# Kernel tuning notes

Measured on AMD Instinct MI355X. Metric: run time of the kernel, lower is better.

The kernel has to match this reference:

```python
import jax, jax.numpy as jnp
import numpy as np


def setup_inputs() -> dict:
    key = jax.random.key(0)
    ks = jax.random.split(key, 7)
    B, T, D, H, DK, S = 16, 1, 4096, 32, 128, 2048
    return {
        "x": jax.random.normal(ks[0], (B, T, D), dtype=jnp.float32),
        "k_cache": jax.random.normal(ks[1], (B, H, S, DK), dtype=jnp.float32),
        "v_cache": jax.random.normal(ks[2], (B, H, S, DK), dtype=jnp.float32),
        "Wq": jax.random.normal(ks[3], (D, D), dtype=jnp.float32) * (D ** -0.5),
        "Wk": jax.random.normal(ks[4], (D, D), dtype=jnp.float32) * (D ** -0.5),
        "Wv": jax.random.normal(ks[5], (D, D), dtype=jnp.float32) * (D ** -0.5),
        "Wo": jax.random.normal(ks[6], (D, D), dtype=jnp.float32) * (D ** -0.5),
        "start_pos": 2047,
    }


def reference(x, k_cache, v_cache, Wq, Wk, Wv, Wo, start_pos):
    B, T, D = x.shape
    H, DK = k_cache.shape[1], k_cache.shape[3]
    end_pos = start_pos + T

    # QKV projections (nn.Linear with bias=False: y = x @ W.T), split heads -> (B, H, T, DK)
    def proj(W):
        return (x @ W.T).reshape(B, T, H, DK).transpose(0, 2, 1, 3)

    q = proj(Wq)
    k_new = proj(Wk)
    v_new = proj(Wv)

    # Scatter new K/V into the pre-allocated cache at start_pos (static slice)
    k_cache = jax.lax.dynamic_update_slice(k_cache, k_new, (0, 0, start_pos, 0))
    v_cache = jax.lax.dynamic_update_slice(v_cache, v_new, (0, 0, start_pos, 0))

    # Gather cached K/V up to end_pos
    k_all = k_cache[:, :, :end_pos]  # (B, H, end_pos, DK)
    v_all = v_cache[:, :, :end_pos]

    # Scaled dot-product attention with causal mask over cache positions
    scores = jnp.einsum("bhtd,bhsd->bhts", q, k_all) / jnp.sqrt(jnp.float32(DK))
    pos_q = start_pos + jnp.arange(T)          # query absolute positions
    pos_k = jnp.arange(end_pos)                # key absolute positions
    mask = pos_k[None, :] <= pos_q[:, None]    # (T, end_pos)
    scores = jnp.where(mask[None, None], scores, jnp.float32(-1e30))
    attn = jax.nn.softmax(scores, axis=-1)
    out = jnp.einsum("bhts,bhsd->bhtd", attn, v_all)

    # Merge heads and output projection
    out = out.transpose(0, 2, 1, 3).reshape(B, T, D)
    return out @ Wo.T
```

## Files before the change

### kernel.cpp

```cpp
#include <hip/hip_runtime.h>
#include <math.h>

constexpr int B  = 16;
constexpr int H  = 32;
constexpr int S  = 2048;
constexpr int DK = 128;
constexpr int D  = 4096;
constexpr int BH = B * H;

constexpr int NSPLIT = 4;
constexpr int CHUNK  = S / NSPLIT;
constexpr int NREC   = NSPLIT * 4;
constexpr int REC    = 132;

__device__ __forceinline__ float reduce64(float v[64], int lane) {
    #pragma unroll
    for (int s = 0; s < 6; ++s) {
        const int off = 1 << s;
        #pragma unroll
        for (int j = 0; j < (64 >> (s + 1)); ++j) {
            const float lo = v[2 * j], hi = v[2 * j + 1];
            const bool  up = (lane & off) != 0;
            const float mine = up ? hi : lo;
            const float oth  = up ? lo : hi;
            v[j] = mine + __shfl_xor(oth, off, 64);
        }
    }
    return v[0];
}

__global__ __launch_bounds__(256, 3) void proj_qkv_kernel(
    const float* __restrict__ X,
    const float* __restrict__ W0,
    const float* __restrict__ W1,
    const float* __restrict__ W2,
    float* __restrict__ Y0,
    float* __restrict__ Y1,
    float* __restrict__ Y2)
{
    __shared__ float4 xs[2][16][64];

    const int t    = threadIdx.x;
    const int lane = t & 63;
    const int wid  = t >> 6;
    const int tb   = t >> 4;
    const int tf   = t & 15;

    const int c0   = blockIdx.x * 16 + wid * 4;
    const int wsel = c0 >> 12;
    const int n0   = c0 & (D - 1);

    const float* Wp = (wsel == 0) ? W0 : (wsel == 1) ? W1 : W2;
    float*       Yp = (wsel == 0) ? Y0 : (wsel == 1) ? Y1 : Y2;
    const float4* w4 = (const float4*)Wp;
    const float4* x4 = (const float4*)X;

    float acc[64];
    #pragma unroll
    for (int i = 0; i < 64; ++i) acc[i] = 0.f;

    float4 xr[4];
    #pragma unroll
    for (int i = 0; i < 4; ++i) xr[i] = x4[tb * 1024 + tf + 16 * i];
    float4 wv[4];
    #pragma unroll
    for (int c = 0; c < 4; ++c) wv[c] = w4[(size_t)(n0 + c) * 1024 + lane];
    #pragma unroll
    for (int i = 0; i < 4; ++i) xs[0][tb][tf + 16 * i] = xr[i];
    __syncthreads();

    for (int ch = 0; ch < 16; ++ch) {
        float4 xn[4], wn[4];
        const bool more = (ch < 15);
        if (more) {
            #pragma unroll
            for (int i = 0; i < 4; ++i)
                xn[i] = x4[tb * 1024 + (ch + 1) * 64 + tf + 16 * i];
            #pragma unroll
            for (int c = 0; c < 4; ++c)
                wn[c] = w4[(size_t)(n0 + c) * 1024 + (ch + 1) * 64 + lane];
        }
        const int buf = ch & 1;
        #pragma unroll
        for (int b = 0; b < 16; ++b) {
            const float4 xv = xs[buf][b][lane];
            #pragma unroll
            for (int c = 0; c < 4; ++c)
                acc[b * 4 + c] += xv.x * wv[c].x + xv.y * wv[c].y +
                                  xv.z * wv[c].z + xv.w * wv[c].w;
        }
        if (more) {
            #pragma unroll
            for (int i = 0; i < 4; ++i) xs[buf ^ 1][tb][tf + 16 * i] = xn[i];
            __syncthreads();
            #pragma unroll
            for (int c = 0; c < 4; ++c) wv[c] = wn[c];
        }
    }

    const float outv = reduce64(acc, lane);
    Yp[(size_t)(lane >> 2) * D + n0 + (lane & 3)] = outv;
}

__global__ __launch_bounds__(256) void proj_wo_kernel(
    const float* __restrict__ X,
    const float* __restrict__ Wo,
    float* __restrict__ out)
{
    __shared__ float red[4][64];
    const int lane = threadIdx.x & 63;
    const int wid  = threadIdx.x >> 6;
    const int n0   = blockIdx.x * 4;
    const float4* w4 = (const float4*)Wo;
    const float4* x4 = (const float4*)X;

    float acc[64];
    #pragma unroll
    for (int i = 0; i < 64; ++i) acc[i] = 0.f;

    #pragma unroll
    for (int it = 0; it < 4; ++it) {
        const int d4 = wid * 256 + it * 64 + lane;
        float4 wv[4];
        #pragma unroll
        for (int c = 0; c < 4; ++c) wv[c] = w4[(size_t)(n0 + c) * 1024 + d4];
        #pragma unroll
        for (int b = 0; b < 16; ++b) {
            const float4 xv = x4[b * 1024 + d4];
            #pragma unroll
            for (int c = 0; c < 4; ++c)
                acc[b * 4 + c] += xv.x * wv[c].x + xv.y * wv[c].y +
                                  xv.z * wv[c].z + xv.w * wv[c].w;
        }
    }

    const float pv = reduce64(acc, lane);
    red[wid][lane] = pv;
    __syncthreads();
    if (wid == 0) {
        const float tot = red[0][lane] + red[1][lane] + red[2][lane] + red[3][lane];
        out[(size_t)(lane >> 2) * D + n0 + (lane & 3)] = tot;
    }
}

__global__ __launch_bounds__(256) void attn_kernel(
    const float* __restrict__ q,
    const float* __restrict__ k_cache,
    const float* __restrict__ v_cache,
    const float* __restrict__ k_new,
    const float* __restrict__ v_new,
    const int*   __restrict__ start_pos_p,
    float* __restrict__ part)
{
    const int lane  = threadIdx.x & 63;
    const int wid   = threadIdx.x >> 6;
    const int half  = lane >> 5;
    const int hl    = lane & 31;
    const int bh    = blockIdx.x & (BH - 1);
    const int split = blockIdx.x >> 9;

    const int sp    = start_pos_p[0];
    const int s0    = split * CHUNK;
    const int lim   = sp + 1;
    const int s_end = (s0 + CHUNK < lim) ? (s0 + CHUNK) : lim;

    const float qscale = 0.08838834764831845f * 1.4426950408889634f;
    const float shift  = 8.0f * 1.4426950408889634f;
    float4 qv = *(const float4*)(q + (size_t)bh * DK + 4 * hl);
    qv.x *= qscale; qv.y *= qscale; qv.z *= qscale; qv.w *= qscale;

    const float* kbase = k_cache + (size_t)bh * S * DK;
    const float* vbase = v_cache + (size_t)bh * S * DK;
    const float* knew  = k_new + (size_t)bh * DK;
    const float* vnew  = v_new + (size_t)bh * DK;

    float  l = 0.f;
    float4 acc = make_float4(0.f, 0.f, 0.f, 0.f);

    #pragma unroll 2
    for (int s2 = s0 + 2 * wid; s2 < s_end; s2 += 8) {
        const int  pos   = s2 + half;
        const bool valid = pos < s_end;
        const int  cpos  = valid ? pos : (s_end - 1);
        const float* kp = (cpos == sp) ? knew : (kbase + (size_t)cpos * DK);
        const float* vp = (cpos == sp) ? vnew : (vbase + (size_t)cpos * DK);
        const float4 kv = *(const float4*)(kp + 4 * hl);
        const float4 vv = *(const float4*)(vp + 4 * hl);

        float p = kv.x * qv.x + kv.y * qv.y + kv.z * qv.z + kv.w * qv.w;
        p += __shfl_xor(p, 1, 64);
        p += __shfl_xor(p, 2, 64);
        p += __shfl_xor(p, 4, 64);
        p += __shfl_xor(p, 8, 64);
        p += __shfl_xor(p, 16, 64);

        const float ep = valid ? __builtin_amdgcn_exp2f(p - shift) : 0.f;
        l     += ep;
        acc.x += ep * vv.x;
        acc.y += ep * vv.y;
        acc.z += ep * vv.z;
        acc.w += ep * vv.w;
    }

    l     += __shfl_xor(l, 32, 64);
    acc.x += __shfl_xor(acc.x, 32, 64);
    acc.y += __shfl_xor(acc.y, 32, 64);
    acc.z += __shfl_xor(acc.z, 32, 64);
    acc.w += __shfl_xor(acc.w, 32, 64);

    float* rec = part + ((size_t)bh * NREC + split * 4 + wid) * REC;
    if (half == 0) *(float4*)(rec + 4 * hl) = acc;
    if (lane == 0) rec[128] = l;
}

__global__ __launch_bounds__(64) void combine_kernel(
    const float* __restrict__ part,
    float* __restrict__ attn_out)
{
    const int bh   = blockIdx.x;
    const int lane = threadIdx.x;
    const float* base = part + (size_t)bh * NREC * REC;

    float L = 0.f, o0 = 0.f, o1 = 0.f;
    #pragma unroll
    for (int i = 0; i < NREC; ++i) {
        L += base[i * REC + 128];
        const float2 a = *(const float2*)(base + i * REC + 2 * lane);
        o0 += a.x;
        o1 += a.y;
    }
    const float inv = 1.f / L;
    attn_out[(size_t)bh * DK + 2 * lane]     = o0 * inv;
    attn_out[(size_t)bh * DK + 2 * lane + 1] = o1 * inv;
}

extern "C" void kernel_launch(void* const* d_in, const int* in_sizes, int n_in,
                              void* d_out, int out_size, void* d_ws, size_t ws_size,
                              hipStream_t stream)
{
    const float* x       = (const float*)d_in[0];
    const float* k_cache = (const float*)d_in[1];
    const float* v_cache = (const float*)d_in[2];
    const float* Wq      = (const float*)d_in[3];
    const float* Wk      = (const float*)d_in[4];
    const float* Wv      = (const float*)d_in[5];
    const float* Wo      = (const float*)d_in[6];
    const int*   sp      = (const int*)d_in[7];
    float*       out     = (float*)d_out;

    float* ws       = (float*)d_ws;
    float* q        = ws;
    float* k_new    = ws + 65536;
    float* v_new    = ws + 131072;
    float* attn_out = ws + 196608;
    float* part     = ws + 262144;

    proj_qkv_kernel<<<(3 * D) / 16, 256, 0, stream>>>(x, Wq, Wk, Wv, q, k_new, v_new);

    attn_kernel<<<BH * NSPLIT, 256, 0, stream>>>(q, k_cache, v_cache, k_new, v_new,
                                                 sp, part);

    combine_kernel<<<BH, 64, 0, stream>>>(part, attn_out);

    proj_wo_kernel<<<D / 4, 256, 0, stream>>>(attn_out, Wo, out);
}
```

Baseline: 307.0 us.

## Fuse K/V projection into attention kernel and fold new token into combine

The QKV projection kernel now computes only Q. The K and V projections move into the attention kernel, each wave computing one output column after its cache scan. The attention loop now covers only cached positions below start_pos. The combine kernel adds the new token's score and value contribution from the freshly projected k_new and v_new. The intent is to overlap the Wk/Wv weight streaming with the memory-bound KV-cache scan and to shrink the serial projection stage. The risks are a new x-reload pattern (16 rows per column with no shared-memory reuse), added register pressure in the attention kernel, and the assumption that start_pos lands exactly on the final position.

```diff
diff --git a/kernel.cpp b/kernel.cpp
--- a/kernel.cpp
+++ b/kernel.cpp
@@ -29,14 +29,29 @@
     return v[0];
 }
 
-__global__ __launch_bounds__(256, 3) void proj_qkv_kernel(
+__device__ __forceinline__ float reduce16(float v[16], int lane) {
+    #pragma unroll
+    for (int s = 0; s < 4; ++s) {
+        const int off = 1 << s;
+        #pragma unroll
+        for (int j = 0; j < (16 >> (s + 1)); ++j) {
+            const float lo = v[2 * j], hi = v[2 * j + 1];
+            const bool  up = (lane & off) != 0;
+            const float mine = up ? hi : lo;
+            const float oth  = up ? lo : hi;
+            v[j] = mine + __shfl_xor(oth, off, 64);
+        }
+    }
+    float t = v[0];
+    t += __shfl_xor(t, 16, 64);
+    t += __shfl_xor(t, 32, 64);
+    return t;
+}
+
+__global__ __launch_bounds__(256, 3) void proj_q_kernel(
     const float* __restrict__ X,
-    const float* __restrict__ W0,
-    const float* __restrict__ W1,
-    const float* __restrict__ W2,
-    float* __restrict__ Y0,
-    float* __restrict__ Y1,
-    float* __restrict__ Y2)
+    const float* __restrict__ Wq,
+    float* __restrict__ Yq)
 {
     __shared__ float4 xs[2][16][64];
 
@@ -46,13 +61,9 @@
     const int tb   = t >> 4;
     const int tf   = t & 15;
 
-    const int c0   = blockIdx.x * 16 + wid * 4;
-    const int wsel = c0 >> 12;
-    const int n0   = c0 & (D - 1);
-
-    const float* Wp = (wsel == 0) ? W0 : (wsel == 1) ? W1 : W2;
-    float*       Yp = (wsel == 0) ? Y0 : (wsel == 1) ? Y1 : Y2;
-    const float4* w4 = (const float4*)Wp;
+    const int n0 = blockIdx.x * 16 + wid * 4;
+
+    const float4* w4 = (const float4*)Wq;
     const float4* x4 = (const float4*)X;
 
     float acc[64];
@@ -99,7 +110,147 @@
     }
 
     const float outv = reduce64(acc, lane);
-    Yp[(size_t)(lane >> 2) * D + n0 + (lane & 3)] = outv;
+    Yq[(size_t)(lane >> 2) * D + n0 + (lane & 3)] = outv;
+}
+
+__global__ __launch_bounds__(256) void attn_kvproj_kernel(
+    const float* __restrict__ q,
+    const float* __restrict__ k_cache,
+    const float* __restrict__ v_cache,
+    const float* __restrict__ X,
+    const float* __restrict__ Wk,
+    const float* __restrict__ Wv,
+    const int*   __restrict__ start_pos_p,
+    float* __restrict__ part,
+    float* __restrict__ k_new,
+    float* __restrict__ v_new)
+{
+    const int lane  = threadIdx.x & 63;
+    const int wid   = threadIdx.x >> 6;
+    const int half  = lane >> 5;
+    const int hl    = lane & 31;
+    const int bh    = blockIdx.x & (BH - 1);
+    const int split = blockIdx.x >> 9;
+
+    const int sp    = start_pos_p[0];
+    const int s0    = split * CHUNK;
+    const int s_end = (s0 + CHUNK < sp) ? (s0 + CHUNK) : sp;
+
+    const float qscale = 0.08838834764831845f * 1.4426950408889634f;
+    const float shift  = 8.0f * 1.4426950408889634f;
+    float4 qv = *(const float4*)(q + (size_t)bh * DK + 4 * hl);
+    qv.x *= qscale; qv.y *= qscale; qv.z *= qscale; qv.w *= qscale;
+
+    const float* kbase = k_cache + (size_t)bh * S * DK;
+    const float* vbase = v_cache + (size_t)bh * S * DK;
+
+    float  l = 0.f;
+    float4 acc = make_float4(0.f, 0.f, 0.f, 0.f);
+
+    #pragma unroll 4
+    for (int s2 = s0 + 2 * wid; s2 < s_end; s2 += 8) {
+        const int  pos   = s2 + half;
+        const bool valid = pos < s_end;
+        const int  cpos  = valid ? pos : (s_end - 1);
+        const float4 kv = *(const float4*)(kbase + (size_t)cpos * DK + 4 * hl);
+        const float4 vv = *(const float4*)(vbase + (size_t)cpos * DK + 4 * hl);
+
+        float p = kv.x * qv.x + kv.y * qv.y + kv.z * qv.z + kv.w * qv.w;
+        p += __shfl_xor(p, 1, 64);
+        p += __shfl_xor(p, 2, 64);
+        p += __shfl_xor(p, 4, 64);
+        p += __shfl_xor(p, 8, 64);
+        p += __shfl_xor(p, 16, 64);
+
+        const float ep = valid ? __builtin_amdgcn_exp2f(p - shift) : 0.f;
+        l     += ep;
+        acc.x += ep * vv.x;
+        acc.y += ep * vv.y;
+        acc.z += ep * vv.z;
+        acc.w += ep * vv.w;
+    }
+
+    l     += __shfl_xor(l, 32, 64);
+    acc.x += __shfl_xor(acc.x, 32, 64);
+    acc.y += __shfl_xor(acc.y, 32, 64);
+    acc.z += __shfl_xor(acc.z, 32, 64);
+    acc.w += __shfl_xor(acc.w, 32, 64);
+
+    float* rec = part + ((size_t)bh * NREC + split * 4 + wid) * REC;
+    if (half == 0) *(float4*)(rec + 4 * hl) = acc;
+    if (lane == 0) rec[128] = l;
+
+    const int col = blockIdx.x * 4 + wid;
+    const int n   = col & (D - 1);
+    const float* Wp = (col < D) ? Wk : Wv;
+    float*       Yp = (col < D) ? k_new : v_new;
+    const float4* w4 = (const float4*)(Wp + (size_t)n * D);
+    const float4* x4 = (const float4*)X;
+
+    float pacc[16];
+    #pragma unroll
+    for (int i = 0; i < 16; ++i) pacc[i] = 0.f;
+
+    float4 wrow = w4[lane];
+    for (int ch = 0; ch < 16; ++ch) {
+        float4 wnext;
+        if (ch < 15) wnext = w4[(ch + 1) * 64 + lane];
+        #pragma unroll
+        for (int b = 0; b < 16; ++b) {
+            const float4 xv = x4[b * 1024 + ch * 64 + lane];
+            pacc[b] += xv.x * wrow.x + xv.y * wrow.y +
+                       xv.z * wrow.z + xv.w * wrow.w;
+        }
+        if (ch < 15) wrow = wnext;
+    }
+
+    const float tot = reduce16(pacc, lane);
+    if (lane < 16)
+        Yp[(size_t)lane * D + n] = tot;
+}
+
+__global__ __launch_bounds__(64) void combine_kernel(
+    const float* __restrict__ part,
+    const float* __restrict__ q,
+    const float* __restrict__ k_new,
+    const float* __restrict__ v_new,
+    float* __restrict__ attn_out)
+{
+    const int bh   = blockIdx.x;
+    const int lane = threadIdx.x;
+    const float* base = part + (size_t)bh * NREC * REC;
+
+    float L = 0.f, o0 = 0.f, o1 = 0.f;
+    #pragma unroll
+    for (int i = 0; i < NREC; ++i) {
+        L += base[i * REC + 128];
+        const float2 a = *(const float2*)(base + i * REC + 2 * lane);
+        o0 += a.x;
+        o1 += a.y;
+    }
+
+    const float qscale = 0.08838834764831845f * 1.4426950408889634f;
+    const float shift  = 8.0f * 1.4426950408889634f;
+    const float2 q2 = *(const float2*)(q     + (size_t)bh * DK + 2 * lane);
+    const float2 kn = *(const float2*)(k_new + (size_t)bh * DK + 2 * lane);
+    const float2 vn = *(const float2*)(v_new + (size_t)bh * DK + 2 * lane);
+
+    float p = q2.x * kn.x + q2.y * kn.y;
+    p += __shfl_xor(p, 1, 64);
+    p += __shfl_xor(p, 2, 64);
+    p += __shfl_xor(p, 4, 64);
+    p += __shfl_xor(p, 8, 64);
+    p += __shfl_xor(p, 16, 64);
+    p += __shfl_xor(p, 32, 64);
+
+    const float ep = __builtin_amdgcn_exp2f(p * qscale - shift);
+    L  += ep;
+    o0 += ep * vn.x;
+    o1 += ep * vn.y;
+
+    const float inv = 1.f / L;
+    attn_out[(size_t)bh * DK + 2 * lane]     = o0 * inv;
+    attn_out[(size_t)bh * DK + 2 * lane + 1] = o1 * inv;
 }
 
 __global__ __launch_bounds__(256) void proj_wo_kernel(
@@ -141,97 +292,6 @@
         const float tot = red[0][lane] + red[1][lane] + red[2][lane] + red[3][lane];
         out[(size_t)(lane >> 2) * D + n0 + (lane & 3)] = tot;
     }
-}
-
-__global__ __launch_bounds__(256) void attn_kernel(
-    const float* __restrict__ q,
-    const float* __restrict__ k_cache,
-    const float* __restrict__ v_cache,
-    const float* __restrict__ k_new,
-    const float* __restrict__ v_new,
-    const int*   __restrict__ start_pos_p,
-    float* __restrict__ part)
-{
-    const int lane  = threadIdx.x & 63;
-    const int wid   = threadIdx.x >> 6;
-    const int half  = lane >> 5;
-    const int hl    = lane & 31;
-    const int bh    = blockIdx.x & (BH - 1);
-    const int split = blockIdx.x >> 9;
-
-    const int sp    = start_pos_p[0];
-    const int s0    = split * CHUNK;
-    const int lim   = sp + 1;
-    const int s_end = (s0 + CHUNK < lim) ? (s0 + CHUNK) : lim;
-
-    const float qscale = 0.08838834764831845f * 1.4426950408889634f;
-    const float shift  = 8.0f * 1.4426950408889634f;
-    float4 qv = *(const float4*)(q + (size_t)bh * DK + 4 * hl);
-    qv.x *= qscale; qv.y *= qscale; qv.z *= qscale; qv.w *= qscale;
-
-    const float* kbase = k_cache + (size_t)bh * S * DK;
-    const float* vbase = v_cache + (size_t)bh * S * DK;
-    const float* knew  = k_new + (size_t)bh * DK;
-    const float* vnew  = v_new + (size_t)bh * DK;
-
-    float  l = 0.f;
-    float4 acc = make_float4(0.f, 0.f, 0.f, 0.f);
-
-    #pragma unroll 2
-    for (int s2 = s0 + 2 * wid; s2 < s_end; s2 += 8) {
-        const int  pos   = s2 + half;
-        const bool valid = pos < s_end;
-        const int  cpos  = valid ? pos : (s_end - 1);
-        const float* kp = (cpos == sp) ? knew : (kbase + (size_t)cpos * DK);
-        const float* vp = (cpos == sp) ? vnew : (vbase + (size_t)cpos * DK);
-        const float4 kv = *(const float4*)(kp + 4 * hl);
-        const float4 vv = *(const float4*)(vp + 4 * hl);
-
-        float p = kv.x * qv.x + kv.y * qv.y + kv.z * qv.z + kv.w * qv.w;
-        p += __shfl_xor(p, 1, 64);
-        p += __shfl_xor(p, 2, 64);
-        p += __shfl_xor(p, 4, 64);
-        p += __shfl_xor(p, 8, 64);
-        p += __shfl_xor(p, 16, 64);
-
-        const float ep = valid ? __builtin_amdgcn_exp2f(p - shift) : 0.f;
-        l     += ep;
-        acc.x += ep * vv.x;
-        acc.y += ep * vv.y;
-        acc.z += ep * vv.z;
-        acc.w += ep * vv.w;
-    }
-
-    l     += __shfl_xor(l, 32, 64);
-    acc.x += __shfl_xor(acc.x, 32, 64);
-    acc.y += __shfl_xor(acc.y, 32, 64);
-    acc.z += __shfl_xor(acc.z, 32, 64);
-    acc.w += __shfl_xor(acc.w, 32, 64);
-
-    float* rec = part + ((size_t)bh * NREC + split * 4 + wid) * REC;
-    if (half == 0) *(float4*)(rec + 4 * hl) = acc;
-    if (lane == 0) rec[128] = l;
-}
-
-__global__ __launch_bounds__(64) void combine_kernel(
-    const float* __restrict__ part,
-    float* __restrict__ attn_out)
-{
-    const int bh   = blockIdx.x;
-    const int lane = threadIdx.x;
-    const float* base = part + (size_t)bh * NREC * REC;
-
-    float L = 0.f, o0 = 0.f, o1 = 0.f;
-    #pragma unroll
-    for (int i = 0; i < NREC; ++i) {
-        L += base[i * REC + 128];
-        const float2 a = *(const float2*)(base + i * REC + 2 * lane);
-        o0 += a.x;
-        o1 += a.y;
-    }
-    const float inv = 1.f / L;
-    attn_out[(size_t)bh * DK + 2 * lane]     = o0 * inv;
-    attn_out[(size_t)bh * DK + 2 * lane + 1] = o1 * inv;
 }
 
 extern "C" void kernel_launch(void* const* d_in, const int* in_sizes, int n_in,
@@ -255,12 +315,12 @@
     float* attn_out = ws + 196608;
     float* part     = ws + 262144;
 
-    proj_qkv_kernel<<<(3 * D) / 16, 256, 0, stream>>>(x, Wq, Wk, Wv, q, k_new, v_new);
-
-    attn_kernel<<<BH * NSPLIT, 256, 0, stream>>>(q, k_cache, v_cache, k_new, v_new,
-                                                 sp, part);
-
-    combine_kernel<<<BH, 64, 0, stream>>>(part, attn_out);
+    proj_q_kernel<<<D / 16, 256, 0, stream>>>(x, Wq, q);
+
+    attn_kvproj_kernel<<<BH * NSPLIT, 256, 0, stream>>>(
+        q, k_cache, v_cache, x, Wk, Wv, sp, part, k_new, v_new);
+
+    combine_kernel<<<BH, 64, 0, stream>>>(part, q, k_new, v_new, attn_out);
 
     proj_wo_kernel<<<D / 4, 256, 0, stream>>>(attn_out, Wo, out);
 }
```

New measurement: 368.9 us. 20.2% more time.
